# Performance work log

Hardware: AMD Instinct MI355X
Metric: run time of the kernel (lower is better)

The kernel has to match this reference:

```python
import jax, jax.numpy as jnp
import numpy as np

B, L, HID, LAT, EXP, NL, H, D = 8, 512, 256, 256, 2, 3, 96, 8
INNER = LAT * EXP


def _layernorm(x, g, b, eps=1e-5):
    mu = x.mean(-1, keepdims=True)
    var = ((x - mu) ** 2).mean(-1, keepdims=True)
    return (x - mu) / jnp.sqrt(var + eps) * g + b


def _rmsnorm(x, w, eps=1e-6):
    return x * jax.lax.rsqrt((x * x).mean(-1, keepdims=True) + eps) * w


def _mamba_block(h, in_w, conv_w, decay, scale, out_w, rms_w):
    # h: [B, L, LAT]
    Lh = h.shape[1]
    xp = h @ in_w                      # [B, L, 2*INNER]
    u, g = jnp.split(xp, 2, axis=-1)   # each [B, L, INNER]
    # causal depthwise conv, kernel 3, left pad 2
    up = jnp.pad(u, ((0, 0), (2, 0), (0, 0)))
    uc = (conv_w[:, 0] * up[:, :Lh]
          + conv_w[:, 1] * up[:, 1:Lh + 1]
          + conv_w[:, 2] * up[:, 2:Lh + 2])
    d = jax.nn.sigmoid(decay)          # [INNER]
    inp = (1.0 - d) * scale * uc       # [B, L, INNER]
    log_d = jnp.log(jnp.clip(d, 1e-6, None))
    t = jnp.arange(Lh, dtype=h.dtype)
    diff = t[:, None] - t[None, :]     # [L, L]
    causal = (diff >= 0).astype(h.dtype)
    # M: [L, L, INNER] quadratic causal decay tensor (as in the torch code)
    M = jnp.exp(jnp.maximum(diff, 0.0)[:, :, None] * log_d) * causal[:, :, None]
    y = jnp.einsum('tkd,bkd->btd', M, inp) * jax.nn.sigmoid(g)
    return _rmsnorm(y @ out_w, rms_w)


def setup_inputs() -> dict:
    key = jax.random.key(0)
    ks = jax.random.split(key, 8)
    s = 0.02
    return {
        'x': jax.random.normal(ks[0], (B, L, HID), jnp.float32),
        'in_proj_w': jax.random.normal(ks[1], (HID, LAT), jnp.float32) * s,
        'in_ln_g': jnp.ones((LAT,), jnp.float32),
        'in_ln_b': jnp.zeros((LAT,), jnp.float32),
        'norms_g': jnp.ones((NL, LAT), jnp.float32),
        'norms_b': jnp.zeros((NL, LAT), jnp.float32),
        'blk_in_w': jax.random.normal(ks[2], (NL, LAT, 2 * INNER), jnp.float32) * s,
        'blk_conv_w': jax.random.normal(ks[3], (NL, INNER, 3), jnp.float32) * s,
        'blk_decay': jnp.zeros((NL, INNER), jnp.float32),
        'blk_scale': jnp.ones((NL, INNER), jnp.float32),
        'blk_out_w': jax.random.normal(ks[4], (NL, INNER, LAT), jnp.float32) * s,
        'blk_rms_w': jnp.ones((NL, LAT), jnp.float32),
        'head_w1': jax.random.normal(ks[5], (LAT, LAT), jnp.float32) * s,
        'head_b1': jnp.zeros((LAT,), jnp.float32),
        'head_ln_g': jnp.ones((LAT,), jnp.float32),
        'head_ln_b': jnp.zeros((LAT,), jnp.float32),
        'head_w2': jax.random.normal(ks[6], (LAT, H * D), jnp.float32) * s,
        'head_b2': jnp.zeros((H * D,), jnp.float32),
        'forecast_horizon': H,
        'input_dim': D,
    }


def reference(x, in_proj_w, in_ln_g, in_ln_b, norms_g, norms_b,
              blk_in_w, blk_conv_w, blk_decay, blk_scale, blk_out_w, blk_rms_w,
              head_w1, head_b1, head_ln_g, head_ln_b, head_w2, head_b2,
              forecast_horizon, input_dim):
    Bx = x.shape[0]
    h = _layernorm(x @ in_proj_w, in_ln_g, in_ln_b)
    for i in range(NL):
        hn = _layernorm(h, norms_g[i], norms_b[i])
        h = h + _mamba_block(hn, blk_in_w[i], blk_conv_w[i], blk_decay[i],
                             blk_scale[i], blk_out_w[i], blk_rms_w[i])
    pooled = h.mean(axis=1) * 0.5 + h[:, -1, :] * 0.5
    z = _layernorm(pooled @ head_w1 + head_b1, head_ln_g, head_ln_b)
    z = jax.nn.gelu(z, approximate=False)  # torch nn.GELU default = exact erf
    out = z @ head_w2 + head_b2            # dropout inactive at eval
    return out.reshape(Bx, forecast_horizon, input_dim)
```

## Files before the change

kernel.cpp:

```cpp
#include <hip/hip_runtime.h>
#include <math.h>


typedef __attribute__((ext_vector_type(8))) __bf16 bf16x8;
typedef __attribute__((ext_vector_type(4))) float f32x4;

__device__ __forceinline__ unsigned short f2b(float f) {
  unsigned int x = __float_as_uint(f);
  unsigned int r = (x + 0x7fffu + ((x >> 16) & 1u)) >> 16;
  return (unsigned short)r;
}

__device__ __forceinline__ void wave_reduce2(float& a, float& b) {
#pragma unroll
  for (int off = 32; off > 0; off >>= 1) {
    a += __shfl_xor(a, off, 64);
    b += __shfl_xor(b, off, 64);
  }
}
__device__ __forceinline__ float wave_reduce1(float a) {
#pragma unroll
  for (int off = 32; off > 0; off >>= 1) a += __shfl_xor(a, off, 64);
  return a;
}

__device__ __forceinline__ bf16x8 cvt8(float4 a, float4 b) {
  bf16x8 r;
  r[0] = (__bf16)a.x; r[1] = (__bf16)a.y; r[2] = (__bf16)a.z; r[3] = (__bf16)a.w;
  r[4] = (__bf16)b.x; r[5] = (__bf16)b.y; r[6] = (__bf16)b.z; r[7] = (__bf16)b.w;
  return r;
}

#define GLD16(gsrc, ldst)                                              \
  __builtin_amdgcn_global_load_lds(                                    \
      (const __attribute__((address_space(1))) void*)(gsrc),           \
      (__attribute__((address_space(3))) void*)(ldst), 16, 0, 0)

__global__ __launch_bounds__(256) void k_setup(
    const float* __restrict__ inproj, const float* __restrict__ binw,
    const float* __restrict__ boutw, unsigned short* __restrict__ inwT,
    unsigned short* __restrict__ binwT, unsigned short* __restrict__ boutwT) {
  __shared__ float t[32][33];
  const int z = blockIdx.z;
  const float* src;
  unsigned short* dst;
  int R, Cc;
  if (z == 0) {
    src = inproj; dst = inwT; R = 256; Cc = 256;
  } else if (z <= 3) {
    src = binw + (size_t)(z - 1) * 256 * 1024;
    dst = binwT + (size_t)(z - 1) * 1024 * 256;
    R = 256; Cc = 1024;
  } else {
    src = boutw + (size_t)(z - 4) * 512 * 256;
    dst = boutwT + (size_t)(z - 4) * 256 * 512;
    R = 512; Cc = 256;
  }
  const int bx = blockIdx.x, by = blockIdx.y;
  if (bx * 32 >= Cc || by * 32 >= R) return;
  const int tx = threadIdx.x & 31, ty = threadIdx.x >> 5;
#pragma unroll
  for (int j = 0; j < 4; ++j)
    t[ty + j * 8][tx] = src[(size_t)(by * 32 + ty + j * 8) * Cc + bx * 32 + tx];
  __syncthreads();
#pragma unroll
  for (int j = 0; j < 4; ++j)
    dst[(size_t)(bx * 32 + ty + j * 8) * R + by * 32 + tx] = f2b(t[tx][ty + j * 8]);
}

template <int KTOT, int MODE, bool AF32>
__global__ __launch_bounds__(256, 2) void k_gemm_epi(
    const void* __restrict__ A, const unsigned short* __restrict__ Bt,
    const float* __restrict__ p1, const float* __restrict__ p2,
    const float* __restrict__ g2, const float* __restrict__ b2,
    float* __restrict__ h, unsigned short* __restrict__ hnb,
    float* __restrict__ part) {
  constexpr int NCH = KTOT / 64;
  constexpr int ABYTES = AF32 ? 4096 : 2048;
  __shared__ __align__(16) unsigned char smem[2 * ABYTES + 2 * 32768];
  __shared__ float ppart[4][256];
  unsigned char* sAb = smem;
  unsigned char* sBb = smem + 2 * ABYTES;
  float* ep = (float*)smem;
  const float* Af = (const float*)A;
  const unsigned short* Ab = (const unsigned short*)A;
  const int tid = threadIdx.x;
  const int lane = tid & 63;
  const int wc = tid >> 6;
  const int bm0 = blockIdx.x * 16;
  const int fr = lane & 15, fg = lane >> 4;

  auto stage = [&](int buf, int c) {
    if (AF32) {
      int row = tid >> 4, p = tid & 15;
      int l = (p & ~7) | ((p & 7) ^ (row & 7));
      GLD16(Af + (size_t)(bm0 + row) * KTOT + c * 64 + l * 4,
            sAb + buf * ABYTES + tid * 16);
    } else {
      if (tid < 128) {
        int row = tid >> 3, p = tid & 7, l = p ^ (row & 7);
        GLD16(Ab + (size_t)(bm0 + row) * KTOT + c * 64 + l * 8,
              sAb + buf * ABYTES + tid * 16);
      }
    }
#pragma unroll
    for (int j = 0; j < 8; ++j) {
      int idx = tid + j * 256;
      int row = idx >> 3, p = idx & 7, l = p ^ (row & 7);
      GLD16(Bt + (size_t)row * KTOT + c * 64 + l * 8, sBb + buf * 32768 + idx * 16);
    }
  };

  f32x4 acc[4] = {};
  stage(0, 0);
  for (int c = 0; c < NCH; ++c) {
    const int cur = c & 1;
    __syncthreads();
    if (c + 1 < NCH) stage(cur ^ 1, c + 1);
#pragma unroll
    for (int kk = 0; kk < 64; kk += 32) {
      bf16x8 af;
      if (AF32) {
        int s0 = (kk >> 2) + fg * 2;
        int p0 = (s0 & ~7) | ((s0 & 7) ^ (fr & 7));
        int s1 = s0 + 1;
        int p1i = (s1 & ~7) | ((s1 & 7) ^ (fr & 7));
        const float* base = (const float*)(sAb + cur * ABYTES) + fr * 64;
        float4 v0 = *(const float4*)(base + p0 * 4);
        float4 v1 = *(const float4*)(base + p1i * 4);
        af = cvt8(v0, v1);
      } else {
        int s = (kk >> 3) + fg;
        int ps = s ^ (fr & 7);
        af = *(const bf16x8*)((const unsigned short*)(sAb + cur * ABYTES) + fr * 64 +
                              ps * 8);
      }
      int sb = (kk >> 3) + fg;
      int pb = sb ^ (fr & 7);
#pragma unroll
      for (int n = 0; n < 4; ++n) {
        const unsigned short* bp = (const unsigned short*)(sBb + cur * 32768) +
                                   (wc * 64 + n * 16 + fr) * 64 + pb * 8;
        acc[n] = __builtin_amdgcn_mfma_f32_16x16x32_bf16(af, *(const bf16x8*)bp,
                                                         acc[n], 0, 0, 0);
      }
    }
  }
  __syncthreads();
#pragma unroll
  for (int n = 0; n < 4; ++n)
#pragma unroll
    for (int j = 0; j < 4; ++j)
      ep[(fg * 4 + j) * 260 + wc * 64 + n * 16 + fr] = acc[n][j];
  __syncthreads();
  const int c0 = lane * 4;
  float4 q1 = *(const float4*)&p1[c0];
  float4 q2v = (MODE == 0) ? *(const float4*)&p2[c0] : float4{0, 0, 0, 0};
  float4 gg2 = (MODE != 2) ? *(const float4*)&g2[c0] : float4{0, 0, 0, 0};
  float4 bb2 = (MODE != 2) ? *(const float4*)&b2[c0] : float4{0, 0, 0, 0};
  float4 psum = {0.f, 0.f, 0.f, 0.f};
#pragma unroll
  for (int r = 0; r < 4; ++r) {
    const int row = wc * 4 + r;
    const size_t grow = (size_t)(bm0 + row) * 256 + c0;
    float4 v = *(const float4*)&ep[row * 260 + c0];
    float4 hh;
    if (MODE == 0) {
      float s = v.x + v.y + v.z + v.w;
      float sq = v.x * v.x + v.y * v.y + v.z * v.z + v.w * v.w;
      wave_reduce2(s, sq);
      float mu = s * (1.f / 256.f);
      float rstd = rsqrtf(sq * (1.f / 256.f) - mu * mu + 1e-5f);
      hh.x = (v.x - mu) * rstd * q1.x + q2v.x;
      hh.y = (v.y - mu) * rstd * q1.y + q2v.y;
      hh.z = (v.z - mu) * rstd * q1.z + q2v.z;
      hh.w = (v.w - mu) * rstd * q1.w + q2v.w;
      *(float4*)&h[grow] = hh;
    } else {
      float sq = v.x * v.x + v.y * v.y + v.z * v.z + v.w * v.w;
      sq = wave_reduce1(sq);
      float rstd = rsqrtf(sq * (1.f / 256.f) + 1e-6f);
      hh = *(const float4*)&h[grow];
      hh.x += v.x * rstd * q1.x;
      hh.y += v.y * rstd * q1.y;
      hh.z += v.z * rstd * q1.z;
      hh.w += v.w * rstd * q1.w;
      *(float4*)&h[grow] = hh;
    }
    if (MODE != 2) {
      float s2 = hh.x + hh.y + hh.z + hh.w;
      float sq2 = hh.x * hh.x + hh.y * hh.y + hh.z * hh.z + hh.w * hh.w;
      wave_reduce2(s2, sq2);
      float mu2 = s2 * (1.f / 256.f);
      float rs2 = rsqrtf(sq2 * (1.f / 256.f) - mu2 * mu2 + 1e-5f);
      ushort4 u;
      u.x = f2b((hh.x - mu2) * rs2 * gg2.x + bb2.x);
      u.y = f2b((hh.y - mu2) * rs2 * gg2.y + bb2.y);
      u.z = f2b((hh.z - mu2) * rs2 * gg2.z + bb2.z);
      u.w = f2b((hh.w - mu2) * rs2 * gg2.w + bb2.w);
      *(ushort4*)&hnb[grow] = u;
    } else {
      psum.x += hh.x;
      psum.y += hh.y;
      psum.z += hh.z;
      psum.w += hh.w;
    }
  }
  if (MODE == 2) {
    *(float4*)&ppart[wc][c0] = psum;
    __syncthreads();
    float pv = ppart[0][tid] + ppart[1][tid] + ppart[2][tid] + ppart[3][tid];
    part[(size_t)blockIdx.x * 256 + tid] = pv;
  }
}

__global__ __launch_bounds__(256) void k_gemm2_scan(
    const unsigned short* __restrict__ A,
    const unsigned short* __restrict__ Bt,
    const float* __restrict__ cw, const float* __restrict__ decay,
    const float* __restrict__ scl, unsigned short* __restrict__ y) {
  __shared__ __align__(16) unsigned char smem[16384 + 2 * 65536];
  unsigned short* sB = (unsigned short*)smem;
  unsigned char* qb = smem + 16384;
  float* su = (float*)(smem + 16384);
  float* sg = su + 8320;
  float* lend = sg + 8320;
  float* carry = lend + 256;
  const int b = blockIdx.y;
  const int d0 = blockIdx.x * 16;
  const int tid = threadIdx.x;
  const int lane = tid & 63;
  const int w = tid >> 6;
  const int fr = lane & 15, fg = lane >> 4;
  const unsigned short* Abp = A + (size_t)b * 512 * 256;

  auto stageQ = [&](int buf, int q) {
#pragma unroll
    for (int j = 0; j < 16; ++j) {
      int idx = tid + j * 256;
      int row = idx >> 3, p = idx & 7, l = p ^ (row & 7);
      GLD16(Abp + (size_t)row * 256 + q * 64 + l * 8, qb + buf * 65536 + idx * 16);
    }
  };
#pragma unroll
  for (int j = 0; j < 4; ++j) {
    int idx = tid + j * 256;
    int row = idx >> 5, p = idx & 31, l = p ^ (row & 7);
    int gr = row < 16 ? d0 + row : 496 + d0 + row;
    GLD16(Bt + (size_t)gr * 256 + l * 8, smem + idx * 16);
  }
  stageQ(0, 0);

  f32x4 au[8] = {}, ag[8] = {};
#pragma unroll
  for (int q = 0; q < 4; ++q) {
    const int cq = q & 1;
    __syncthreads();
    if (q < 3) stageQ(cq ^ 1, q + 1);
#pragma unroll
    for (int kk = 0; kk < 64; kk += 32) {
      int lb = q * 8 + (kk >> 3) + fg;
      int pb = lb ^ (fr & 7);
      bf16x8 bu = *(const bf16x8*)&sB[fr * 256 + pb * 8];
      bf16x8 bg = *(const bf16x8*)&sB[(16 + fr) * 256 + pb * 8];
      int pa = ((kk >> 3) + fg) ^ (fr & 7);
#pragma unroll
      for (int m = 0; m < 8; ++m) {
        int row = w * 128 + m * 16 + fr;
        bf16x8 af =
            *(const bf16x8*)((const unsigned short*)(qb + cq * 65536) + row * 64 +
                             pa * 8);
        au[m] = __builtin_amdgcn_mfma_f32_16x16x32_bf16(af, bu, au[m], 0, 0, 0);
        ag[m] = __builtin_amdgcn_mfma_f32_16x16x32_bf16(af, bg, ag[m], 0, 0, 0);
      }
    }
  }
  __syncthreads();
#pragma unroll
  for (int m = 0; m < 8; ++m)
#pragma unroll
    for (int j = 0; j < 4; ++j) {
      int row = w * 128 + m * 16 + fg * 4 + j;
      int off = (row >> 5) * 520 + (row & 31) * 16 + fr;
      su[off] = au[m][j];
      sg[off] = ag[m][j];
    }
  __syncthreads();
  const int ds = tid & 15, ch = tid >> 4;
  const int d = d0 + ds;
  const float a = 1.f / (1.f + __expf(-decay[d]));
  const float coef = (1.f - a) * scl[d];
  const float cw0 = cw[d * 3], cw1 = cw[d * 3 + 1], cw2 = cw[d * 3 + 2];
  const int T0 = ch * 32;
  float um1 = T0 >= 1 ? su[((T0 - 1) >> 5) * 520 + ((T0 - 1) & 31) * 16 + ds] : 0.f;
  float um2 = T0 >= 2 ? su[((T0 - 2) >> 5) * 520 + ((T0 - 2) & 31) * 16 + ds] : 0.f;
  float s = 0.f, s0r[32];
#pragma unroll
  for (int t = 0; t < 32; ++t) {
    float u = su[ch * 520 + t * 16 + ds];
    float uc = fmaf(cw0, um2, fmaf(cw1, um1, cw2 * u));
    s = fmaf(a, s, coef * uc);
    s0r[t] = s;
    um2 = um1;
    um1 = u;
  }
  lend[ch * 16 + ds] = s;
  __syncthreads();
  if (tid < 16) {
    float aa = 1.f / (1.f + __expf(-decay[d0 + tid]));
    float a32 = aa * aa;
    a32 = a32 * a32;
    a32 = a32 * a32;
    a32 = a32 * a32;
    a32 = a32 * a32;
    float c = 0.f;
#pragma unroll
    for (int j = 0; j < 16; ++j) {
      carry[j * 16 + tid] = c;
      c = fmaf(a32, c, lend[j * 16 + tid]);
    }
  }
  __syncthreads();
  const float c = carry[ch * 16 + ds];
  unsigned short* yp = y + ((size_t)b * 512 + T0) * 512 + d;
  float ap = a;
#pragma unroll
  for (int t = 0; t < 32; ++t) {
    float gv = sg[ch * 520 + t * 16 + ds];
    float sv = fmaf(ap, c, s0r[t]);
    float sig = 1.f / (1.f + __expf(-gv));
    yp[(size_t)t * 512] = f2b(sv * sig);
    ap *= a;
  }
}

__global__ __launch_bounds__(1024) void k_head(
    const float* __restrict__ part, const float* __restrict__ h,
    const float* __restrict__ w1, const float* __restrict__ b1,
    const float* __restrict__ lng, const float* __restrict__ lnb,
    const float* __restrict__ w2, const float* __restrict__ b2,
    float* __restrict__ out) {
  const int b = blockIdx.x;
  const int t = threadIdx.x;
  const int ks = threadIdx.y;
  __shared__ float sp[256];
  __shared__ float sz[256];
  __shared__ float part4[4][256];
  __shared__ float red[8];
  if (ks == 0) {
    float s = 0.f;
#pragma unroll
    for (int j = 0; j < 32; ++j) s += part[((size_t)b * 32 + j) * 256 + t];
    sp[t] = s * (0.5f / 512.f) + 0.5f * h[(((size_t)b * 512) + 511) * 256 + t];
  }
  __syncthreads();
  float acc = 0.f;
#pragma unroll 8
  for (int k = ks * 64; k < ks * 64 + 64; ++k) acc += sp[k] * w1[(size_t)k * 256 + t];
  part4[ks][t] = acc;
  __syncthreads();
  if (ks == 0) {
    float aval = part4[0][t] + part4[1][t] + part4[2][t] + part4[3][t] + b1[t];
    float s = aval, sq = aval * aval;
    wave_reduce2(s, sq);
    const int lane = t & 63, w = t >> 6;
    if (lane == 0) {
      red[w] = s;
      red[4 + w] = sq;
    }
    part4[0][t] = aval;
  }
  __syncthreads();
  if (ks == 0) {
    float S = red[0] + red[1] + red[2] + red[3];
    float SQ = red[4] + red[5] + red[6] + red[7];
    float mu = S * (1.f / 256.f);
    float rstd = rsqrtf(SQ * (1.f / 256.f) - mu * mu + 1e-5f);
    float zv = (part4[0][t] - mu) * rstd * lng[t] + lnb[t];
    zv = 0.5f * zv * (1.f + erff(zv * 0.70710678118654752f));
    sz[t] = zv;
  }
  __syncthreads();
  const int col = ks * 256 + t;
  if (col < 768) {
    float a = b2[col];
#pragma unroll 8
    for (int k = 0; k < 256; ++k) a += sz[k] * w2[(size_t)k * 768 + col];
    out[(size_t)b * 768 + col] = a;
  }
}

extern "C" void kernel_launch(void* const* d_in, const int* in_sizes, int n_in,
                              void* d_out, int out_size, void* d_ws, size_t ws_size,
                              hipStream_t stream) {
  const float* x = (const float*)d_in[0];
  const float* in_proj_w = (const float*)d_in[1];
  const float* in_ln_g = (const float*)d_in[2];
  const float* in_ln_b = (const float*)d_in[3];
  const float* norms_g = (const float*)d_in[4];
  const float* norms_b = (const float*)d_in[5];
  const float* blk_in_w = (const float*)d_in[6];
  const float* blk_conv_w = (const float*)d_in[7];
  const float* blk_decay = (const float*)d_in[8];
  const float* blk_scale = (const float*)d_in[9];
  const float* blk_out_w = (const float*)d_in[10];
  const float* blk_rms_w = (const float*)d_in[11];
  const float* head_w1 = (const float*)d_in[12];
  const float* head_b1 = (const float*)d_in[13];
  const float* head_ln_g = (const float*)d_in[14];
  const float* head_ln_b = (const float*)d_in[15];
  const float* head_w2 = (const float*)d_in[16];
  const float* head_b2 = (const float*)d_in[17];

  char* wsb = (char*)d_ws;
  float* h = (float*)(wsb + 0);
  float* part = (float*)(wsb + (4 << 20));
  unsigned short* hnb = (unsigned short*)(wsb + (8 << 20));
  unsigned short* yb = (unsigned short*)(wsb + (12 << 20));
  unsigned short* inwT = (unsigned short*)(wsb + (25 << 20));
  unsigned short* binwT = inwT + 65536;
  unsigned short* boutwT = binwT + 786432;
  float* out = (float*)d_out;

  k_setup<<<dim3(32, 16, 7), 256, 0, stream>>>(in_proj_w, blk_in_w, blk_out_w, inwT,
                                               binwT, boutwT);
  k_gemm_epi<256, 0, true><<<256, 256, 0, stream>>>(
      x, inwT, in_ln_g, in_ln_b, norms_g, norms_b, h, hnb, nullptr);
  for (int i = 0; i < 3; ++i) {
    k_gemm2_scan<<<dim3(32, 8), 256, 0, stream>>>(
        hnb, binwT + (size_t)i * 262144, blk_conv_w + i * 1536, blk_decay + i * 512,
        blk_scale + i * 512, yb);
    if (i < 2)
      k_gemm_epi<512, 1, false><<<256, 256, 0, stream>>>(
          yb, boutwT + (size_t)i * 131072, blk_rms_w + i * 256, nullptr,
          norms_g + (i + 1) * 256, norms_b + (i + 1) * 256, h, hnb, nullptr);
    else
      k_gemm_epi<512, 2, false><<<256, 256, 0, stream>>>(
          yb, boutwT + (size_t)i * 131072, blk_rms_w + i * 256, nullptr, nullptr,
          nullptr, h, nullptr, part);
  }
  k_head<<<8, dim3(256, 4), 0, stream>>>(part, h, head_w1, head_b1, head_ln_g,
                                         head_ln_b, head_w2, head_b2, out);
}
```

Before: 101.8 us.

## Enlarge GEMM-epilogue row tile to 64 rows and restructure head kernel

The GEMM+norm epilogue kernel now computes 64 rows per block instead of 16, with a 4x4 MFMA accumulator grid per wave. The goal is to reuse each staged B tile across four times as many rows and cut redundant weight traffic, at the cost of only 64 blocks on a many-CU GPU and higher register/LDS use. The head kernel is split into 24 blocks of 256 threads, each redoing the first projection and LayerNorm and computing one third of the output columns. The partial-sum count in the head drops from 32 to 8 to match the new grid.

```diff
diff --git a/kernel.cpp b/kernel.cpp
--- a/kernel.cpp
+++ b/kernel.cpp
@@ -69,14 +69,14 @@
 }
 
 template <int KTOT, int MODE, bool AF32>
-__global__ __launch_bounds__(256, 2) void k_gemm_epi(
+__global__ __launch_bounds__(256) void k_gemm_epi(
     const void* __restrict__ A, const unsigned short* __restrict__ Bt,
     const float* __restrict__ p1, const float* __restrict__ p2,
     const float* __restrict__ g2, const float* __restrict__ b2,
     float* __restrict__ h, unsigned short* __restrict__ hnb,
     float* __restrict__ part) {
   constexpr int NCH = KTOT / 64;
-  constexpr int ABYTES = AF32 ? 4096 : 2048;
+  constexpr int ABYTES = AF32 ? 16384 : 8192;
   __shared__ __align__(16) unsigned char smem[2 * ABYTES + 2 * 32768];
   __shared__ float ppart[4][256];
   unsigned char* sAb = smem;
@@ -87,20 +87,26 @@
   const int tid = threadIdx.x;
   const int lane = tid & 63;
   const int wc = tid >> 6;
-  const int bm0 = blockIdx.x * 16;
+  const int bm0 = blockIdx.x * 64;
   const int fr = lane & 15, fg = lane >> 4;
 
   auto stage = [&](int buf, int c) {
     if (AF32) {
-      int row = tid >> 4, p = tid & 15;
-      int l = (p & ~7) | ((p & 7) ^ (row & 7));
-      GLD16(Af + (size_t)(bm0 + row) * KTOT + c * 64 + l * 4,
-            sAb + buf * ABYTES + tid * 16);
+#pragma unroll
+      for (int j = 0; j < 4; ++j) {
+        int idx = tid + j * 256;
+        int row = idx >> 4, p = idx & 15;
+        int l = (p & ~7) | ((p & 7) ^ (row & 7));
+        GLD16(Af + (size_t)(bm0 + row) * KTOT + c * 64 + l * 4,
+              sAb + buf * ABYTES + idx * 16);
+      }
     } else {
-      if (tid < 128) {
-        int row = tid >> 3, p = tid & 7, l = p ^ (row & 7);
+#pragma unroll
+      for (int j = 0; j < 2; ++j) {
+        int idx = tid + j * 256;
+        int row = idx >> 3, p = idx & 7, l = p ^ (row & 7);
         GLD16(Ab + (size_t)(bm0 + row) * KTOT + c * 64 + l * 8,
-              sAb + buf * ABYTES + tid * 16);
+              sAb + buf * ABYTES + idx * 16);
       }
     }
 #pragma unroll
@@ -111,7 +117,7 @@
     }
   };
 
-  f32x4 acc[4] = {};
+  f32x4 acc[4][4] = {};
   stage(0, 0);
   for (int c = 0; c < NCH; ++c) {
     const int cur = c & 1;
@@ -119,39 +125,46 @@
     if (c + 1 < NCH) stage(cur ^ 1, c + 1);
 #pragma unroll
     for (int kk = 0; kk < 64; kk += 32) {
-      bf16x8 af;
-      if (AF32) {
-        int s0 = (kk >> 2) + fg * 2;
-        int p0 = (s0 & ~7) | ((s0 & 7) ^ (fr & 7));
-        int s1 = s0 + 1;
-        int p1i = (s1 & ~7) | ((s1 & 7) ^ (fr & 7));
-        const float* base = (const float*)(sAb + cur * ABYTES) + fr * 64;
-        float4 v0 = *(const float4*)(base + p0 * 4);
-        float4 v1 = *(const float4*)(base + p1i * 4);
-        af = cvt8(v0, v1);
-      } else {
-        int s = (kk >> 3) + fg;
-        int ps = s ^ (fr & 7);
-        af = *(const bf16x8*)((const unsigned short*)(sAb + cur * ABYTES) + fr * 64 +
-                              ps * 8);
+      bf16x8 bf[4];
+      const int sb = (kk >> 3) + fg;
+      const int pb = sb ^ (fr & 7);
+#pragma unroll
+      for (int n = 0; n < 4; ++n) {
+        int brow = wc * 64 + n * 16 + fr;
+        bf[n] = *(const bf16x8*)((const unsigned short*)(sBb + cur * 32768) +
+                                 brow * 64 + pb * 8);
       }
-      int sb = (kk >> 3) + fg;
-      int pb = sb ^ (fr & 7);
-#pragma unroll
-      for (int n = 0; n < 4; ++n) {
-        const unsigned short* bp = (const unsigned short*)(sBb + cur * 32768) +
-                                   (wc * 64 + n * 16 + fr) * 64 + pb * 8;
-        acc[n] = __builtin_amdgcn_mfma_f32_16x16x32_bf16(af, *(const bf16x8*)bp,
-                                                         acc[n], 0, 0, 0);
+#pragma unroll
+      for (int m = 0; m < 4; ++m) {
+        bf16x8 af;
+        const int arow = m * 16 + fr;
+        if (AF32) {
+          int s0 = (kk >> 2) + fg * 2;
+          int p0 = (s0 & ~7) | ((s0 & 7) ^ (fr & 7));
+          int s1 = s0 + 1;
+          int p1i = (s1 & ~7) | ((s1 & 7) ^ (fr & 7));
+          const float* base = (const float*)(sAb + cur * ABYTES) + arow * 64;
+          af = cvt8(*(const float4*)(base + p0 * 4), *(const float4*)(base + p1i * 4));
+        } else {
+          int ps = ((kk >> 3) + fg) ^ (fr & 7);
+          af = *(const bf16x8*)((const unsigned short*)(sAb + cur * ABYTES) +
+                                arow * 64 + ps * 8);
+        }
+#pragma unroll
+        for (int n = 0; n < 4; ++n)
+          acc[m][n] = __builtin_amdgcn_mfma_f32_16x16x32_bf16(af, bf[n], acc[m][n],
+                                                              0, 0, 0);
       }
     }
   }
   __syncthreads();
 #pragma unroll
-  for (int n = 0; n < 4; ++n)
-#pragma unroll
-    for (int j = 0; j < 4; ++j)
-      ep[(fg * 4 + j) * 260 + wc * 64 + n * 16 + fr] = acc[n][j];
+  for (int m = 0; m < 4; ++m)
+#pragma unroll
+    for (int n = 0; n < 4; ++n)
+#pragma unroll
+      for (int j = 0; j < 4; ++j)
+        ep[(m * 16 + fg * 4 + j) * 260 + wc * 64 + n * 16 + fr] = acc[m][n][j];
   __syncthreads();
   const int c0 = lane * 4;
   float4 q1 = *(const float4*)&p1[c0];
@@ -160,8 +173,8 @@
   float4 bb2 = (MODE != 2) ? *(const float4*)&b2[c0] : float4{0, 0, 0, 0};
   float4 psum = {0.f, 0.f, 0.f, 0.f};
 #pragma unroll
-  for (int r = 0; r < 4; ++r) {
-    const int row = wc * 4 + r;
+  for (int r = 0; r < 16; ++r) {
+    const int row = wc * 16 + r;
     const size_t grow = (size_t)(bm0 + row) * 256 + c0;
     float4 v = *(const float4*)&ep[row * 260 + c0];
     float4 hh;
@@ -267,9 +280,8 @@
 #pragma unroll
       for (int m = 0; m < 8; ++m) {
         int row = w * 128 + m * 16 + fr;
-        bf16x8 af =
-            *(const bf16x8*)((const unsigned short*)(qb + cq * 65536) + row * 64 +
-                             pa * 8);
+        bf16x8 af = *(const bf16x8*)((const unsigned short*)(qb + cq * 65536) +
+                                     row * 64 + pa * 8);
         au[m] = __builtin_amdgcn_mfma_f32_16x16x32_bf16(af, bu, au[m], 0, 0, 0);
         ag[m] = __builtin_amdgcn_mfma_f32_16x16x32_bf16(af, bg, ag[m], 0, 0, 0);
       }
@@ -334,60 +346,46 @@
   }
 }
 
-__global__ __launch_bounds__(1024) void k_head(
+__global__ __launch_bounds__(256) void k_head(
     const float* __restrict__ part, const float* __restrict__ h,
     const float* __restrict__ w1, const float* __restrict__ b1,
     const float* __restrict__ lng, const float* __restrict__ lnb,
     const float* __restrict__ w2, const float* __restrict__ b2,
     float* __restrict__ out) {
-  const int b = blockIdx.x;
-  const int t = threadIdx.x;
-  const int ks = threadIdx.y;
+  const int b = blockIdx.x / 3, j3 = blockIdx.x % 3;
+  const int tid = threadIdx.x;
   __shared__ float sp[256];
   __shared__ float sz[256];
-  __shared__ float part4[4][256];
   __shared__ float red[8];
-  if (ks == 0) {
-    float s = 0.f;
-#pragma unroll
-    for (int j = 0; j < 32; ++j) s += part[((size_t)b * 32 + j) * 256 + t];
-    sp[t] = s * (0.5f / 512.f) + 0.5f * h[(((size_t)b * 512) + 511) * 256 + t];
-  }
-  __syncthreads();
-  float acc = 0.f;
+  float s = 0.f;
+#pragma unroll
+  for (int j = 0; j < 8; ++j) s += part[((size_t)b * 8 + j) * 256 + tid];
+  sp[tid] = s * (0.5f / 512.f) + 0.5f * h[(((size_t)b * 512) + 511) * 256 + tid];
+  __syncthreads();
+  float acc = b1[tid];
 #pragma unroll 8
-  for (int k = ks * 64; k < ks * 64 + 64; ++k) acc += sp[k] * w1[(size_t)k * 256 + t];
-  part4[ks][t] = acc;
-  __syncthreads();
-  if (ks == 0) {
-    float aval = part4[0][t] + part4[1][t] + part4[2][t] + part4[3][t] + b1[t];
-    float s = aval, sq = aval * aval;
-    wave_reduce2(s, sq);
-    const int lane = t & 63, w = t >> 6;
-    if (lane == 0) {
-      red[w] = s;
-      red[4 + w] = sq;
-    }
-    part4[0][t] = aval;
-  }
-  __syncthreads();
-  if (ks == 0) {
-    float S = red[0] + red[1] + red[2] + red[3];
-    float SQ = red[4] + red[5] + red[6] + red[7];
-    float mu = S * (1.f / 256.f);
-    float rstd = rsqrtf(SQ * (1.f / 256.f) - mu * mu + 1e-5f);
-    float zv = (part4[0][t] - mu) * rstd * lng[t] + lnb[t];
-    zv = 0.5f * zv * (1.f + erff(zv * 0.70710678118654752f));
-    sz[t] = zv;
-  }
-  __syncthreads();
-  const int col = ks * 256 + t;
-  if (col < 768) {
-    float a = b2[col];
+  for (int k = 0; k < 256; ++k) acc += sp[k] * w1[(size_t)k * 256 + tid];
+  float ss = acc, sq = acc * acc;
+  wave_reduce2(ss, sq);
+  const int lane = tid & 63, w = tid >> 6;
+  if (lane == 0) {
+    red[w] = ss;
+    red[4 + w] = sq;
+  }
+  __syncthreads();
+  float S = red[0] + red[1] + red[2] + red[3];
+  float SQ = red[4] + red[5] + red[6] + red[7];
+  float mu = S * (1.f / 256.f);
+  float rstd = rsqrtf(SQ * (1.f / 256.f) - mu * mu + 1e-5f);
+  float zv = (acc - mu) * rstd * lng[tid] + lnb[tid];
+  zv = 0.5f * zv * (1.f + erff(zv * 0.70710678118654752f));
+  sz[tid] = zv;
+  __syncthreads();
+  const int col = j3 * 256 + tid;
+  float a = b2[col];
 #pragma unroll 8
-    for (int k = 0; k < 256; ++k) a += sz[k] * w2[(size_t)k * 768 + col];
-    out[(size_t)b * 768 + col] = a;
-  }
+  for (int k = 0; k < 256; ++k) a += sz[k] * w2[(size_t)k * 768 + col];
+  out[(size_t)b * 768 + col] = a;
 }
 
 extern "C" void kernel_launch(void* const* d_in, const int* in_sizes, int n_in,
@@ -424,21 +422,21 @@
 
   k_setup<<<dim3(32, 16, 7), 256, 0, stream>>>(in_proj_w, blk_in_w, blk_out_w, inwT,
                                                binwT, boutwT);
-  k_gemm_epi<256, 0, true><<<256, 256, 0, stream>>>(
+  k_gemm_epi<256, 0, true><<<64, 256, 0, stream>>>(
       x, inwT, in_ln_g, in_ln_b, norms_g, norms_b, h, hnb, nullptr);
   for (int i = 0; i < 3; ++i) {
     k_gemm2_scan<<<dim3(32, 8), 256, 0, stream>>>(
         hnb, binwT + (size_t)i * 262144, blk_conv_w + i * 1536, blk_decay + i * 512,
         blk_scale + i * 512, yb);
     if (i < 2)
-      k_gemm_epi<512, 1, false><<<256, 256, 0, stream>>>(
+      k_gemm_epi<512, 1, false><<<64, 256, 0, stream>>>(
           yb, boutwT + (size_t)i * 131072, blk_rms_w + i * 256, nullptr,
           norms_g + (i + 1) * 256, norms_b + (i + 1) * 256, h, hnb, nullptr);
     else
-      k_gemm_epi<512, 2, false><<<256, 256, 0, stream>>>(
+      k_gemm_epi<512, 2, false><<<64, 256, 0, stream>>>(
           yb, boutwT + (size_t)i * 131072, blk_rms_w + i * 256, nullptr, nullptr,
           nullptr, h, nullptr, part);
   }
-  k_head<<<8, dim3(256, 4), 0, stream>>>(part, h, head_w1, head_b1, head_ln_g,
-                                         head_ln_b, head_w2, head_b2, out);
-}
+  k_head<<<24, 256, 0, stream>>>(part, h, head_w1, head_b1, head_ln_g, head_ln_b,
+                                 head_w2, head_b2, out);
+}
```

After: 125.6 us. 23.4% more time.
